# Kernel optimization log

Hardware: AMD Instinct MI355X
Metric: run time of the kernel (lower is better)

The kernel has to match this reference:

```python
import jax, jax.numpy as jnp
import numpy as np
import math

N = 16384        # nodes / rows of inputs
DIN = 256        # input_dimension
DOUT = 64        # output_dimension (contraction dim of second matmul)
M = 16384        # columns of normalized_adjacency (output width)


def setup_inputs() -> dict:
    key = jax.random.key(0)
    k1, k2, k3 = jax.random.split(key, 3)
    inputs = jax.random.normal(k1, (N, DIN), dtype=jnp.float32)
    normalized_adjacency = jax.random.uniform(k2, (DOUT, M), dtype=jnp.float32)
    dev = 1.0 / math.sqrt(DOUT)  # Xavier-style uniform init from source
    weights = jax.random.uniform(k3, (DIN, DOUT), dtype=jnp.float32,
                                 minval=-dev, maxval=dev)
    return {"inputs": inputs, "normalized_adjacency": normalized_adjacency,
            "weights": weights}


def reference(inputs, normalized_adjacency, weights):
    # before = X @ W : [N, DOUT]
    before = jnp.matmul(inputs, weights)
    # returning = before @ A : [N, M]  (spmm in source; same math densely)
    returning = jnp.matmul(before, normalized_adjacency)
    # bias=0 => no bias add; torch legacy softmax on 2-D uses dim=1
    return jax.nn.softmax(returning, axis=-1)
```

## Files before the change

### kernel.cpp

```cpp
#include <hip/hip_runtime.h>
#include <hip/hip_bf16.h>

#define N_ROWS 16384
#define DIN_K  256
#define DOUT_K 64
#define M_COLS 16384
#define LOG2E  1.4426950408889634f

typedef __attribute__((ext_vector_type(8))) short short8;
typedef __attribute__((ext_vector_type(4))) float f32x4;

#define MFMA16 __builtin_amdgcn_mfma_f32_16x16x32_bf16
#define EXP2F  __builtin_amdgcn_exp2f
#define LOG2F  __builtin_amdgcn_logf

__device__ inline unsigned short f32_bf16_rne(float x) {
    unsigned u = __builtin_bit_cast(unsigned, x);
    u += 0x7fffu + ((u >> 16) & 1u);
    return (unsigned short)(u >> 16);
}
__device__ inline float bf16_f32(unsigned short h) {
    unsigned u = ((unsigned)h) << 16;
    return __builtin_bit_cast(float, u);
}

__global__ __launch_bounds__(256) void k_before(
    const float* __restrict__ X, const float* __restrict__ W,
    float* __restrict__ off2,
    unsigned short* __restrict__ bh, unsigned short* __restrict__ bl)
{
    const int row  = blockIdx.x * 4 + (threadIdx.x >> 6);
    const int lane = threadIdx.x & 63;
    const float* xr = X + (size_t)row * DIN_K;
    float acc = 0.f;
    #pragma unroll 8
    for (int d = 0; d < DIN_K; ++d)
        acc = fmaf(xr[d], W[d * DOUT_K + lane], acc);
    const float bs = acc * LOG2E;
    const unsigned short hs = f32_bf16_rne(bs);
    const float hf = bf16_f32(hs);
    const unsigned short ls = f32_bf16_rne(bs - hf);
    bh[row * DOUT_K + lane] = hs;
    bl[row * DOUT_K + lane] = ls;
    float t = fmaxf(bs, 0.f);
    #pragma unroll
    for (int m = 1; m < 64; m <<= 1) t += __shfl_xor(t, m, 64);
    if (lane == 0) off2[row] = t;
}

__global__ __launch_bounds__(256) void k_pack(
    const float* __restrict__ A,
    unsigned short* __restrict__ ahp, unsigned short* __restrict__ alp)
{
    const int wid   = blockIdx.x * 4 + (threadIdx.x >> 6);
    const int lane  = threadIdx.x & 63;
    const int chunk = wid >> 1, ks = wid & 1;
    const int col   = chunk * 16 + (lane & 15);
    const int kb    = ks * 32 + ((lane >> 4) * 8);
    const size_t base = ((size_t)(chunk * 2 + ks) * 64 + lane) * 8;
    #pragma unroll
    for (int i = 0; i < 8; ++i) {
        const float a = A[(size_t)(kb + i) * M_COLS + col];
        const unsigned short hs = f32_bf16_rne(a);
        ahp[base + i] = hs;
        alp[base + i] = f32_bf16_rne(a - bf16_f32(hs));
    }
}

__global__ __launch_bounds__(512, 2) void k_main(
    const unsigned short* __restrict__ bh, const unsigned short* __restrict__ bl,
    const unsigned short* __restrict__ ahp, const unsigned short* __restrict__ alp,
    const float* __restrict__ off2, float* __restrict__ out)
{
    __shared__ float lds[8][64];
    __shared__ float sout[64 * 260];
    const int wave = threadIdx.x >> 6;
    const int lane = threadIdx.x & 63;
    const int lrow = lane & 15;
    const int lgrp = lane >> 4;
    const int r0   = blockIdx.x * 64;
    const int rot  = (((blockIdx.x << 3) | wave) * 53) & 127;
    const int cbase = wave * 128;

#define CIDX(j) (cbase + (((j) + rot) & 127))

    short8 bHf[4][2], bLf[4][2];
    #pragma unroll
    for (int rt = 0; rt < 4; ++rt)
        #pragma unroll
        for (int ks = 0; ks < 2; ++ks) {
            const size_t o = (size_t)(r0 + rt * 16 + lrow) * DOUT_K + ks * 32 + lgrp * 8;
            bHf[rt][ks] = *reinterpret_cast<const short8*>(bh + o);
            bLf[rt][ks] = *reinterpret_cast<const short8*>(bl + o);
        }

    float negoff[4];
    #pragma unroll
    for (int rt = 0; rt < 4; ++rt)
        negoff[rt] = -off2[r0 + rt * 16 + lrow];

    float lsum[4] = {0.f, 0.f, 0.f, 0.f};

#define LOADA(H0, H1, c) {                                                  \
    const size_t _b = (size_t)((c) * 2) * 512 + lane * 8;                   \
    H0 = *reinterpret_cast<const short8*>(ahp + _b);                        \
    H1 = *reinterpret_cast<const short8*>(ahp + _b + 512); }

#define LOADB(H0, H1, L0, L1, c) {                                          \
    const size_t _b = (size_t)((c) * 2) * 512 + lane * 8;                   \
    H0 = *reinterpret_cast<const short8*>(ahp + _b);                        \
    H1 = *reinterpret_cast<const short8*>(ahp + _b + 512);                  \
    L0 = *reinterpret_cast<const short8*>(alp + _b);                        \
    L1 = *reinterpret_cast<const short8*>(alp + _b + 512); }

#define BODY1(H0, H1)                                                       \
    _Pragma("unroll")                                                       \
    for (int rt = 0; rt < 4; ++rt) {                                        \
        f32x4 acc = { negoff[rt], negoff[rt], negoff[rt], negoff[rt] };     \
        acc = MFMA16(H0, bHf[rt][0], acc, 0, 0, 0);                         \
        acc = MFMA16(H1, bHf[rt][1], acc, 0, 0, 0);                         \
        acc = MFMA16(H0, bLf[rt][0], acc, 0, 0, 0);                         \
        acc = MFMA16(H1, bLf[rt][1], acc, 0, 0, 0);                         \
        lsum[rt] += (EXP2F(acc[0]) + EXP2F(acc[1]))                         \
                  + (EXP2F(acc[2]) + EXP2F(acc[3])); }

    short8 cH0, cH1, nH0, nH1;

    LOADA(cH0, cH1, CIDX(0));
    for (int j = 0; j < 128; j += 2) {
        LOADA(nH0, nH1, CIDX(j + 1));
        BODY1(cH0, cH1);
        LOADA(cH0, cH1, CIDX(j + 2));
        BODY1(nH0, nH1);
    }

    #pragma unroll
    for (int rt = 0; rt < 4; ++rt) {
        float v = lsum[rt];
        v += __shfl_xor(v, 16, 64);
        v += __shfl_xor(v, 32, 64);
        lsum[rt] = v;
    }
    if (lgrp == 0) {
        #pragma unroll
        for (int rt = 0; rt < 4; ++rt)
            lds[wave][rt * 16 + lrow] = lsum[rt];
    }
    __syncthreads();

    float base2[4];
    #pragma unroll
    for (int rt = 0; rt < 4; ++rt) {
        const int rl = rt * 16 + lrow;
        float tot = ((lds[0][rl] + lds[1][rl]) + (lds[2][rl] + lds[3][rl]))
                  + ((lds[4][rl] + lds[5][rl]) + (lds[6][rl] + lds[7][rl]));
        base2[rt] = negoff[rt] - LOG2F(tot);
    }

    const int rotb = (blockIdx.x * 37) & 63;
    const int k0 = wave * 2, k1 = wave * 2 + 1;

#define LOADPAIR(H00,H01,L00,L01, H10,H11,L10,L11, sp) {                    \
    const int _cc = (sp) * 16 + k0;                                         \
    LOADB(H00, H01, L00, L01, _cc);                                         \
    LOADB(H10, H11, L10, L11, _cc + 1); }

#define BODY2L(H0, H1, L0, L1, kk)                                          \
    _Pragma("unroll")                                                       \
    for (int rt = 0; rt < 4; ++rt) {                                        \
        f32x4 acc = { base2[rt], base2[rt], base2[rt], base2[rt] };         \
        acc = MFMA16(H0, bHf[rt][0], acc, 0, 0, 0);                         \
        acc = MFMA16(H1, bHf[rt][1], acc, 0, 0, 0);                         \
        acc = MFMA16(L0, bHf[rt][0], acc, 0, 0, 0);                         \
        acc = MFMA16(L1, bHf[rt][1], acc, 0, 0, 0);                         \
        acc = MFMA16(H0, bLf[rt][0], acc, 0, 0, 0);                         \
        acc = MFMA16(H1, bLf[rt][1], acc, 0, 0, 0);                         \
        f32x4 o4 = { EXP2F(acc[0]), EXP2F(acc[1]),                          \
                     EXP2F(acc[2]), EXP2F(acc[3]) };                        \
        *reinterpret_cast<f32x4*>(                                          \
            &sout[(rt * 16 + lrow) * 260 + (kk) * 16 + lgrp * 4]) = o4; }

#define STOREPHASE(sp) {                                                    \
    const size_t _cb = (size_t)(sp) * 256;                                  \
    _Pragma("unroll")                                                       \
    for (int i = 0; i < 8; ++i) {                                           \
        const int _rw = wave * 8 + i;                                       \
        const f32x4 v = *reinterpret_cast<const f32x4*>(                    \
            &sout[_rw * 260 + lane * 4]);                                   \
        __builtin_nontemporal_store(v, reinterpret_cast<f32x4*>(            \
            out + (size_t)(r0 + _rw) * M_COLS + _cb + lane * 4)); } }

    short8 A0H0,A0H1,A0L0,A0L1, A1H0,A1H1,A1L0,A1L1;
    short8 B0H0,B0H1,B0L0,B0L1, B1H0,B1H1,B1L0,B1L1;

    LOADPAIR(A0H0,A0H1,A0L0,A0L1, A1H0,A1H1,A1L0,A1L1, rotb);
    for (int s = 0; s < 64; s += 2) {
        const int spE = (s + rotb) & 63;
        const int spO = (s + 1 + rotb) & 63;
        const int spN = (s + 2 + rotb) & 63;
        BODY2L(A0H0,A0H1,A0L0,A0L1, k0);
        BODY2L(A1H0,A1H1,A1L0,A1L1, k1);
        LOADPAIR(B0H0,B0H1,B0L0,B0L1, B1H0,B1H1,B1L0,B1L1, spO);
        __syncthreads();
        STOREPHASE(spE);
        __syncthreads();
        BODY2L(B0H0,B0H1,B0L0,B0L1, k0);
        BODY2L(B1H0,B1H1,B1L0,B1L1, k1);
        LOADPAIR(A0H0,A0H1,A0L0,A0L1, A1H0,A1H1,A1L0,A1L1, spN);
        __syncthreads();
        STOREPHASE(spO);
        __syncthreads();
    }
#undef CIDX
#undef LOADA
#undef LOADB
#undef BODY1
#undef LOADPAIR
#undef BODY2L
#undef STOREPHASE
}

extern "C" void kernel_launch(void* const* d_in, const int* in_sizes, int n_in,
                              void* d_out, int out_size, void* d_ws, size_t ws_size,
                              hipStream_t stream) {
    const float* X = (const float*)d_in[0];
    const float* A = (const float*)d_in[1];
    const float* W = (const float*)d_in[2];
    float* out = (float*)d_out;

    char* wsb = (char*)d_ws;
    float*          off2 = (float*)wsb;
    unsigned short* bh   = (unsigned short*)(wsb + (1u << 16));
    unsigned short* bl   = (unsigned short*)(wsb + (1u << 16) + (1u << 21));
    unsigned short* ahp  = (unsigned short*)(wsb + (1u << 16) + 2u * (1u << 21));
    unsigned short* alp  = (unsigned short*)(wsb + (1u << 16) + 3u * (1u << 21));

    hipLaunchKernelGGL(k_before, dim3(N_ROWS / 4), dim3(256), 0, stream, X, W, off2, bh, bl);
    hipLaunchKernelGGL(k_pack,   dim3(512),        dim3(256), 0, stream, A, ahp, alp);
    hipLaunchKernelGGL(k_main,   dim3(256),        dim3(512), 0, stream, bh, bl, ahp, alp, off2, out);
}
```

Before: 307.5 us.

## Double-buffer LDS output staging to overlap stores with MFMA compute

Splits the shared-memory output tile into two buffers so that one phase's results are written to global memory while the next phase is computed into the other buffer. This cuts the barriers per phase pair from four to two and lets global stores overlap MFMA and exp work. The cost is doubled LDS usage per block, which likely limits the kernel to one resident block per CU instead of two.

```diff
diff --git a/kernel.cpp b/kernel.cpp
--- a/kernel.cpp
+++ b/kernel.cpp
@@ -73,7 +73,8 @@
     const float* __restrict__ off2, float* __restrict__ out)
 {
     __shared__ float lds[8][64];
-    __shared__ float sout[64 * 260];
+    __shared__ float sout0[64 * 260];
+    __shared__ float sout1[64 * 260];
     const int wave = threadIdx.x >> 6;
     const int lane = threadIdx.x & 63;
     const int lrow = lane & 15;
@@ -165,7 +166,7 @@
     LOADB(H00, H01, L00, L01, _cc);                                         \
     LOADB(H10, H11, L10, L11, _cc + 1); }
 
-#define BODY2L(H0, H1, L0, L1, kk)                                          \
+#define BODY2L(H0, H1, L0, L1, kk, BUF)                                     \
     _Pragma("unroll")                                                       \
     for (int rt = 0; rt < 4; ++rt) {                                        \
         f32x4 acc = { base2[rt], base2[rt], base2[rt], base2[rt] };         \
@@ -178,15 +179,15 @@
         f32x4 o4 = { EXP2F(acc[0]), EXP2F(acc[1]),                          \
                      EXP2F(acc[2]), EXP2F(acc[3]) };                        \
         *reinterpret_cast<f32x4*>(                                          \
-            &sout[(rt * 16 + lrow) * 260 + (kk) * 16 + lgrp * 4]) = o4; }
-
-#define STOREPHASE(sp) {                                                    \
+            &BUF[(rt * 16 + lrow) * 260 + (kk) * 16 + lgrp * 4]) = o4; }
+
+#define STOREPHASE(sp, BUF) {                                               \
     const size_t _cb = (size_t)(sp) * 256;                                  \
     _Pragma("unroll")                                                       \
     for (int i = 0; i < 8; ++i) {                                           \
         const int _rw = wave * 8 + i;                                       \
         const f32x4 v = *reinterpret_cast<const f32x4*>(                    \
-            &sout[_rw * 260 + lane * 4]);                                   \
+            &BUF[_rw * 260 + lane * 4]);                                    \
         __builtin_nontemporal_store(v, reinterpret_cast<f32x4*>(            \
             out + (size_t)(r0 + _rw) * M_COLS + _cb + lane * 4)); } }
 
@@ -194,23 +195,30 @@
     short8 B0H0,B0H1,B0L0,B0L1, B1H0,B1H1,B1L0,B1L1;
 
     LOADPAIR(A0H0,A0H1,A0L0,A0L1, A1H0,A1H1,A1L0,A1L1, rotb);
-    for (int s = 0; s < 64; s += 2) {
+    BODY2L(A0H0,A0H1,A0L0,A0L1, k0, sout0);
+    BODY2L(A1H0,A1H1,A1L0,A1L1, k1, sout0);
+    LOADPAIR(B0H0,B0H1,B0L0,B0L1, B1H0,B1H1,B1L0,B1L1, (1 + rotb) & 63);
+    __syncthreads();
+
+    for (int s = 0; s < 62; s += 2) {
         const int spE = (s + rotb) & 63;
         const int spO = (s + 1 + rotb) & 63;
-        const int spN = (s + 2 + rotb) & 63;
-        BODY2L(A0H0,A0H1,A0L0,A0L1, k0);
-        BODY2L(A1H0,A1H1,A1L0,A1L1, k1);
-        LOADPAIR(B0H0,B0H1,B0L0,B0L1, B1H0,B1H1,B1L0,B1L1, spO);
+        STOREPHASE(spE, sout0);
+        LOADPAIR(A0H0,A0H1,A0L0,A0L1, A1H0,A1H1,A1L0,A1L1, (s + 2 + rotb) & 63);
+        BODY2L(B0H0,B0H1,B0L0,B0L1, k0, sout1);
+        BODY2L(B1H0,B1H1,B1L0,B1L1, k1, sout1);
         __syncthreads();
-        STOREPHASE(spE);
+        STOREPHASE(spO, sout1);
+        LOADPAIR(B0H0,B0H1,B0L0,B0L1, B1H0,B1H1,B1L0,B1L1, (s + 3 + rotb) & 63);
+        BODY2L(A0H0,A0H1,A0L0,A0L1, k0, sout0);
+        BODY2L(A1H0,A1H1,A1L0,A1L1, k1, sout0);
         __syncthreads();
-        BODY2L(B0H0,B0H1,B0L0,B0L1, k0);
-        BODY2L(B1H0,B1H1,B1L0,B1L1, k1);
-        LOADPAIR(A0H0,A0H1,A0L0,A0L1, A1H0,A1H1,A1L0,A1L1, spN);
-        __syncthreads();
-        STOREPHASE(spO);
-        __syncthreads();
-    }
+    }
+    STOREPHASE((62 + rotb) & 63, sout0);
+    BODY2L(B0H0,B0H1,B0L0,B0L1, k0, sout1);
+    BODY2L(B1H0,B1H1,B1L0,B1L1, k1, sout1);
+    __syncthreads();
+    STOREPHASE((63 + rotb) & 63, sout1);
 #undef CIDX
 #undef LOADA
 #undef LOADB
```

New measurement: 307.9 us (median of 2 runs). About the same (+0.1%).
